# Kernel optimization log

Measured on AMD Instinct MI355X. Metric: run time of the kernel, lower is better.

## Reference

```python
import jax, jax.numpy as jnp
import numpy as np

B, L, D = 1, 256, 256
H, DK, R = 8, 32, 2
EPS = 1e-6


def _proj_ode(x, t, W, b, r):
    """Stand-in for ODELinear/InterpLinear: linear projection of x broadcast
    over a second time index with r exponential time-decay coefficients.
    x: [B,L,D], t: [B,L] -> [B,L,L,r,D_out]"""
    base = x @ W.T + b                                  # [B,L,Do]
    dt = jnp.abs(t[:, :, None] - t[:, None, :])         # [B,L,L]
    steps = jnp.linspace(0.0, 1.0, r, dtype=x.dtype)    # [r]
    coef = jnp.exp(-dt[:, :, :, None] * steps)          # [B,L,L,r]
    return coef[..., None] * base[:, None, :, None, :]  # [B,L,L,r,Do]


def _layer_norm(x, g, b):
    mu = x.mean(-1, keepdims=True)
    var = ((x - mu) ** 2).mean(-1, keepdims=True)
    return (x - mu) * jax.lax.rsqrt(var + EPS) * g + b


def setup_inputs() -> dict:
    key = jax.random.key(0)
    ks = jax.random.split(key, 12)
    s = 1.0 / np.sqrt(D)
    return {
        "q": jax.random.normal(ks[0], (B, L, D), jnp.float32),
        "k": jax.random.normal(ks[1], (B, L, D), jnp.float32),
        "v": jax.random.normal(ks[2], (B, L, D), jnp.float32),
        "t": jax.random.uniform(ks[3], (B, L), jnp.float32),
        "Wq": jax.random.normal(ks[4], (D, D), jnp.float32) * s,
        "bq": jnp.zeros((D,), jnp.float32),
        "Wk": jax.random.normal(ks[5], (D, D), jnp.float32) * s,
        "bk": jnp.zeros((D,), jnp.float32),
        "Wv": jax.random.normal(ks[6], (D, D), jnp.float32) * s,
        "bv": jnp.zeros((D,), jnp.float32),
        "fc_w": jax.random.normal(ks[7], (D, D), jnp.float32) * s,
        "fc_b": jnp.zeros((D,), jnp.float32),
        "ln_g": jnp.ones((D,), jnp.float32),
        "ln_b": jnp.zeros((D,), jnp.float32),
    }


def reference(q, k, v, t, Wq, bq, Wk, bk, Wv, bv, fc_w, fc_b, ln_g, ln_b):
    temp = DK ** 0.5
    residual = q
    qn = _layer_norm(q, ln_g, ln_b)  # normalize_before=True (only q)

    # [B,L,L,R,D] -> [B,L,L,R,H,DK] -> [B,H,L,L,R,DK]
    def to6(x):
        return x.reshape(B, L, L, R, H, DK).transpose(0, 4, 1, 2, 3, 5)

    qp = to6(_proj_ode(qn, t, Wq, bq, R))
    kp = to6(_proj_ode(k, t, Wk, bk, R))
    vp = to6(_proj_ode(v, t, Wv, bv, R))

    # attn = (q/temp * k).sum(-1).sum(-1): multiply-reduce over (R, DK), no matmul
    attn = jnp.einsum('bhijrd,bhijrd->bhij', qp, kp) / temp
    attn = jax.nn.softmax(attn, axis=-1)  # dropout=0 (eval)

    vs = vp.sum(axis=4)                                   # reduce R: [B,H,L,L,DK]
    out = jnp.einsum('bhij,bhijd->bhid', attn, vs)        # reduce second L
    out = out.transpose(0, 2, 1, 3).reshape(B, L, H * DK)
    out = out @ fc_w.T + fc_b
    out = out + residual
    return (out, attn)
```

## Files before the change

### kernel.cpp

```cpp
#include <hip/hip_runtime.h>
#include <math.h>


#define INV_TEMP 0.17677669529663687f

__device__ __forceinline__ void gemm_panel(
    const float* __restrict__ X, const float* __restrict__ W,
    const float* __restrict__ bias, const float* __restrict__ res,
    const float* __restrict__ ln_g, const float* __restrict__ ln_b,
    float* __restrict__ out, const int mode) {
  __shared__ float As[256][36];
  __shared__ float Bs[256][36];
  __shared__ float Red[4][32][36];
  const int t = threadIdx.x;
  const int j0 = blockIdx.y << 5, o0 = blockIdx.x << 5;
  const int lr = t >> 3;
  const int cg = (t & 7) << 2;
  float4 xa[8], wb[8];
#pragma unroll
  for (int u = 0; u < 8; ++u) {
    xa[u] = *(const float4*)(X + ((j0 + lr) << 8) + (u << 5) + cg);
    wb[u] = *(const float4*)(W + ((o0 + lr) << 8) + (u << 5) + cg);
  }
  if (mode == 0) {
    float s = 0.f, s2 = 0.f;
#pragma unroll
    for (int u = 0; u < 8; ++u) {
      s  += xa[u].x + xa[u].y + xa[u].z + xa[u].w;
      s2 += xa[u].x * xa[u].x + xa[u].y * xa[u].y +
            xa[u].z * xa[u].z + xa[u].w * xa[u].w;
    }
#pragma unroll
    for (int off = 1; off < 8; off <<= 1) {
      s  += __shfl_xor(s, off);
      s2 += __shfl_xor(s2, off);
    }
    const float mu = s * 0.00390625f;
    const float rs = rsqrtf(s2 * 0.00390625f - mu * mu + 1e-6f);
#pragma unroll
    for (int u = 0; u < 8; ++u) {
      const float4 gv = *(const float4*)(ln_g + (u << 5) + cg);
      const float4 bv = *(const float4*)(ln_b + (u << 5) + cg);
      xa[u].x = (xa[u].x - mu) * rs * gv.x + bv.x;
      xa[u].y = (xa[u].y - mu) * rs * gv.y + bv.y;
      xa[u].z = (xa[u].z - mu) * rs * gv.z + bv.z;
      xa[u].w = (xa[u].w - mu) * rs * gv.w + bv.w;
    }
  }
#pragma unroll
  for (int u = 0; u < 8; ++u) {
    const int c = (u << 5) + cg;
    As[c + 0][lr] = xa[u].x; As[c + 1][lr] = xa[u].y;
    As[c + 2][lr] = xa[u].z; As[c + 3][lr] = xa[u].w;
    Bs[c + 0][lr] = wb[u].x; Bs[c + 1][lr] = wb[u].y;
    Bs[c + 2][lr] = wb[u].z; Bs[c + 3][lr] = wb[u].w;
  }
  __syncthreads();

  const int w = t >> 6, lane = t & 63;
  const int jb = (lane >> 3) << 2;
  const int ob = (lane & 7) << 2;
  const int kbase = w << 6;
  float acc[4][4] = {{0.f}};
#pragma unroll 8
  for (int kk = 0; kk < 64; ++kk) {
    const float4 av = *(const float4*)&As[kbase + kk][jb];
    const float4 bv = *(const float4*)&Bs[kbase + kk][ob];
    acc[0][0] = fmaf(av.x, bv.x, acc[0][0]);
    acc[0][1] = fmaf(av.x, bv.y, acc[0][1]);
    acc[0][2] = fmaf(av.x, bv.z, acc[0][2]);
    acc[0][3] = fmaf(av.x, bv.w, acc[0][3]);
    acc[1][0] = fmaf(av.y, bv.x, acc[1][0]);
    acc[1][1] = fmaf(av.y, bv.y, acc[1][1]);
    acc[1][2] = fmaf(av.y, bv.z, acc[1][2]);
    acc[1][3] = fmaf(av.y, bv.w, acc[1][3]);
    acc[2][0] = fmaf(av.z, bv.x, acc[2][0]);
    acc[2][1] = fmaf(av.z, bv.y, acc[2][1]);
    acc[2][2] = fmaf(av.z, bv.z, acc[2][2]);
    acc[2][3] = fmaf(av.z, bv.w, acc[2][3]);
    acc[3][0] = fmaf(av.w, bv.x, acc[3][0]);
    acc[3][1] = fmaf(av.w, bv.y, acc[3][1]);
    acc[3][2] = fmaf(av.w, bv.z, acc[3][2]);
    acc[3][3] = fmaf(av.w, bv.w, acc[3][3]);
  }
#pragma unroll
  for (int r = 0; r < 4; ++r)
    *(float4*)&Red[w][jb + r][ob] =
        make_float4(acc[r][0], acc[r][1], acc[r][2], acc[r][3]);
  __syncthreads();

  const int j = t >> 3, o4 = (t & 7) << 2;
  const float4 s0 = *(const float4*)&Red[0][j][o4];
  const float4 s1 = *(const float4*)&Red[1][j][o4];
  const float4 s2 = *(const float4*)&Red[2][j][o4];
  const float4 s3 = *(const float4*)&Red[3][j][o4];
  const float4 bv4 = *(const float4*)(bias + o0 + o4);
  float4 rs4;
  rs4.x = (s0.x + s1.x) + (s2.x + s3.x) + bv4.x;
  rs4.y = (s0.y + s1.y) + (s2.y + s3.y) + bv4.y;
  rs4.z = (s0.z + s1.z) + (s2.z + s3.z) + bv4.z;
  rs4.w = (s0.w + s1.w) + (s2.w + s3.w) + bv4.w;
  const int gj = j0 + j, go = o0 + o4;
  if (mode <= 1) {
    out[((go + 0) << 8) + gj] = rs4.x;
    out[((go + 1) << 8) + gj] = rs4.y;
    out[((go + 2) << 8) + gj] = rs4.z;
    out[((go + 3) << 8) + gj] = rs4.w;
  } else {
    if (mode == 3) {
      const float4 rv = *(const float4*)(res + (gj << 8) + go);
      rs4.x += rv.x; rs4.y += rv.y; rs4.z += rv.z; rs4.w += rv.w;
    }
    *(float4*)(out + (gj << 8) + go) = rs4;
  }
}

__global__ __launch_bounds__(256) void mha_proj_gemm3(
    const float* __restrict__ q, const float* __restrict__ kin,
    const float* __restrict__ vin, const float* __restrict__ Wq,
    const float* __restrict__ bq, const float* __restrict__ Wk,
    const float* __restrict__ bk, const float* __restrict__ Wv,
    const float* __restrict__ bv, const float* __restrict__ ln_g,
    const float* __restrict__ ln_b, float* __restrict__ baseQT,
    float* __restrict__ baseKT, float* __restrict__ baseV) {
  const int z = blockIdx.z;
  if (z == 0)
    gemm_panel(q, Wq, bq, nullptr, ln_g, ln_b, baseQT, 0);
  else if (z == 1)
    gemm_panel(kin, Wk, bk, nullptr, nullptr, nullptr, baseKT, 1);
  else
    gemm_panel(vin, Wv, bv, nullptr, nullptr, nullptr, baseV, 2);
}

__global__ __launch_bounds__(256) void mha_fc_gemm(
    const float* __restrict__ ctxf, const float* __restrict__ fc_w,
    const float* __restrict__ fc_b, const float* __restrict__ q,
    float* __restrict__ out) {
  gemm_panel(ctxf, fc_w, fc_b, q, nullptr, nullptr, out, 3);
}

__global__ __launch_bounds__(512) void mha_attn_fused(
    const float* __restrict__ baseQT, const float* __restrict__ baseKT,
    const float* __restrict__ baseV, const float* __restrict__ tt,
    float* __restrict__ attn_out, float* __restrict__ ctxf) {
  const int h = blockIdx.y;
  const int i0 = blockIdx.x << 3;
  const int t = threadIdx.x;
  __shared__ float s_lds[256];
  __shared__ float P[8][256];
  if (t < 256) {
    const float* qc = baseQT + (h << 13) + t;
    const float* kc = baseKT + (h << 13) + t;
    float acc = 0.f;
#pragma unroll
    for (int dk = 0; dk < 32; ++dk)
      acc = fmaf(qc[dk << 8], kc[dk << 8], acc);
    s_lds[t] = acc * INV_TEMP;
  }
  __syncthreads();

  const int w = t >> 6, lane = t & 63;
  const int i = i0 + w;
  const float ti = tt[i];
  const float4 tj = ((const float4*)tt)[lane];
  const float4 sv = ((const float4*)s_lds)[lane];
  const float e0 = __expf(-fabsf(ti - tj.x));
  const float e1 = __expf(-fabsf(ti - tj.y));
  const float e2 = __expf(-fabsf(ti - tj.z));
  const float e3 = __expf(-fabsf(ti - tj.w));
  const float sc0 = (1.f + e0 * e0) * sv.x;
  const float sc1 = (1.f + e1 * e1) * sv.y;
  const float sc2 = (1.f + e2 * e2) * sv.z;
  const float sc3 = (1.f + e3 * e3) * sv.w;
  float m = fmaxf(fmaxf(sc0, sc1), fmaxf(sc2, sc3));
#pragma unroll
  for (int off = 32; off; off >>= 1) m = fmaxf(m, __shfl_xor(m, off));
  float p0 = __expf(sc0 - m), p1 = __expf(sc1 - m);
  float p2 = __expf(sc2 - m), p3 = __expf(sc3 - m);
  float s = p0 + p1 + p2 + p3;
#pragma unroll
  for (int off = 32; off; off >>= 1) s += __shfl_xor(s, off);
  const float rinv = 1.f / s;
  p0 *= rinv; p1 *= rinv; p2 *= rinv; p3 *= rinv;
  ((float4*)(attn_out + (((h << 8) + i) << 8)))[lane] =
      make_float4(p0, p1, p2, p3);
  ((float4*)P[w])[lane] = make_float4(p0 * (1.f + e0), p1 * (1.f + e1),
                                      p2 * (1.f + e2), p3 * (1.f + e3));

  const int dk = lane & 31, half = lane >> 5;
  const float* Pr = P[w] + (half << 7);
  const float* Vp = baseV + (h << 5) + dk + (half << 15);
  float a0 = 0.f, a1 = 0.f, a2 = 0.f, a3 = 0.f;
#pragma unroll 4
  for (int jj = 0; jj < 128; jj += 4) {
    a0 = fmaf(Pr[jj + 0], Vp[(jj + 0) << 8], a0);
    a1 = fmaf(Pr[jj + 1], Vp[(jj + 1) << 8], a1);
    a2 = fmaf(Pr[jj + 2], Vp[(jj + 2) << 8], a2);
    a3 = fmaf(Pr[jj + 3], Vp[(jj + 3) << 8], a3);
  }
  float acc = (a0 + a1) + (a2 + a3);
  acc += __shfl_xor(acc, 32);
  if (half == 0) ctxf[(i << 8) + (h << 5) + dk] = acc;
}

extern "C" void kernel_launch(void* const* d_in, const int* in_sizes, int n_in,
                              void* d_out, int out_size, void* d_ws,
                              size_t ws_size, hipStream_t stream) {
  const float* q    = (const float*)d_in[0];
  const float* kin  = (const float*)d_in[1];
  const float* vin  = (const float*)d_in[2];
  const float* tt   = (const float*)d_in[3];
  const float* Wq   = (const float*)d_in[4];
  const float* bq   = (const float*)d_in[5];
  const float* Wk   = (const float*)d_in[6];
  const float* bk   = (const float*)d_in[7];
  const float* Wv   = (const float*)d_in[8];
  const float* bv   = (const float*)d_in[9];
  const float* fc_w = (const float*)d_in[10];
  const float* fc_b = (const float*)d_in[11];
  const float* ln_g = (const float*)d_in[12];
  const float* ln_b = (const float*)d_in[13];

  float* out  = (float*)d_out;
  float* attn = out + 65536;

  float* ws     = (float*)d_ws;
  float* baseQT = ws;
  float* baseKT = ws + 65536;
  float* baseV  = ws + 131072;
  float* ctxf   = ws + 196608;

  hipLaunchKernelGGL(mha_proj_gemm3, dim3(8, 8, 3), dim3(256), 0, stream, q,
                     kin, vin, Wq, bq, Wk, bk, Wv, bv, ln_g, ln_b, baseQT,
                     baseKT, baseV);
  hipLaunchKernelGGL(mha_attn_fused, dim3(32, 8), dim3(512), 0, stream,
                     baseQT, baseKT, baseV, tt, attn, ctxf);
  hipLaunchKernelGGL(mha_fc_gemm, dim3(8, 8), dim3(256), 0, stream, ctxf,
                     fc_w, fc_b, q, out);
}
```

Baseline: 96.54 us.

## Fuse output projection into attention kernel with per-head atomic accumulation

Removes the separate fc GEMM launch. Each attention block now multiplies its per-head context slice by the matching rows of a transposed fc_w and atomically adds the partial result into the output. Head 0 also adds the bias and the residual. The projection kernel now zeroes the output and writes the fc_w transpose, so no extra launch is needed for that setup. This saves one kernel launch and the ctx round-trip through global memory. In exchange it adds eight float atomics per output element, which makes the summation order nondeterministic.

Measured after the change: 103.1 us. +6.8%, slower.

```diff
diff --git a/kernel.cpp b/kernel.cpp
--- a/kernel.cpp
+++ b/kernel.cpp
@@ -6,9 +6,8 @@
 
 __device__ __forceinline__ void gemm_panel(
     const float* __restrict__ X, const float* __restrict__ W,
-    const float* __restrict__ bias, const float* __restrict__ res,
-    const float* __restrict__ ln_g, const float* __restrict__ ln_b,
-    float* __restrict__ out, const int mode) {
+    const float* __restrict__ bias, const float* __restrict__ ln_g,
+    const float* __restrict__ ln_b, float* __restrict__ out, const int mode) {
   __shared__ float As[256][36];
   __shared__ float Bs[256][36];
   __shared__ float Red[4][32][36];
@@ -107,10 +106,6 @@
     out[((go + 2) << 8) + gj] = rs4.z;
     out[((go + 3) << 8) + gj] = rs4.w;
   } else {
-    if (mode == 3) {
-      const float4 rv = *(const float4*)(res + (gj << 8) + go);
-      rs4.x += rv.x; rs4.y += rv.y; rs4.z += rv.z; rs4.w += rv.w;
-    }
     *(float4*)(out + (gj << 8) + go) = rs4;
   }
 }
@@ -121,33 +116,45 @@
     const float* __restrict__ bq, const float* __restrict__ Wk,
     const float* __restrict__ bk, const float* __restrict__ Wv,
     const float* __restrict__ bv, const float* __restrict__ ln_g,
-    const float* __restrict__ ln_b, float* __restrict__ baseQT,
-    float* __restrict__ baseKT, float* __restrict__ baseV) {
+    const float* __restrict__ ln_b, const float* __restrict__ fc_w,
+    float* __restrict__ baseQT, float* __restrict__ baseKT,
+    float* __restrict__ baseV, float* __restrict__ fc_wT,
+    float* __restrict__ outz) {
   const int z = blockIdx.z;
+  const int gid = ((z << 6) + (blockIdx.y << 3) + blockIdx.x) * 256 +
+                  threadIdx.x;
+  if (gid < 16384)
+    ((float4*)outz)[gid] = make_float4(0.f, 0.f, 0.f, 0.f);
+  {
+    const int e = gid << 1;
+    if (e < 65536) {
+      const float2 v = *(const float2*)(fc_w + e);
+      const int o = e >> 8, d = e & 255;
+      fc_wT[(d << 8) + o] = v.x;
+      fc_wT[((d + 1 < 256 ? d + 1 : d - 255) << 8) +
+            (d + 1 < 256 ? o : o + 1)] = v.y;
+    }
+  }
   if (z == 0)
-    gemm_panel(q, Wq, bq, nullptr, ln_g, ln_b, baseQT, 0);
+    gemm_panel(q, Wq, bq, ln_g, ln_b, baseQT, 0);
   else if (z == 1)
-    gemm_panel(kin, Wk, bk, nullptr, nullptr, nullptr, baseKT, 1);
+    gemm_panel(kin, Wk, bk, nullptr, nullptr, baseKT, 1);
   else
-    gemm_panel(vin, Wv, bv, nullptr, nullptr, nullptr, baseV, 2);
-}
-
-__global__ __launch_bounds__(256) void mha_fc_gemm(
-    const float* __restrict__ ctxf, const float* __restrict__ fc_w,
-    const float* __restrict__ fc_b, const float* __restrict__ q,
-    float* __restrict__ out) {
-  gemm_panel(ctxf, fc_w, fc_b, q, nullptr, nullptr, out, 3);
-}
-
-__global__ __launch_bounds__(512) void mha_attn_fused(
+    gemm_panel(vin, Wv, bv, nullptr, nullptr, baseV, 2);
+}
+
+__global__ __launch_bounds__(512) void mha_attn_fc(
     const float* __restrict__ baseQT, const float* __restrict__ baseKT,
     const float* __restrict__ baseV, const float* __restrict__ tt,
-    float* __restrict__ attn_out, float* __restrict__ ctxf) {
+    const float* __restrict__ fc_wT, const float* __restrict__ fc_b,
+    const float* __restrict__ qres, float* __restrict__ attn_out,
+    float* __restrict__ out) {
   const int h = blockIdx.y;
   const int i0 = blockIdx.x << 3;
   const int t = threadIdx.x;
   __shared__ float s_lds[256];
   __shared__ float P[8][256];
+  __shared__ float ctx_lds[8][32];
   if (t < 256) {
     const float* qc = baseQT + (h << 13) + t;
     const float* kc = baseKT + (h << 13) + t;
@@ -200,7 +207,39 @@
   }
   float acc = (a0 + a1) + (a2 + a3);
   acc += __shfl_xor(acc, 32);
-  if (half == 0) ctxf[(i << 8) + (h << 5) + dk] = acc;
+  if (half == 0) ctx_lds[w][dk] = acc;
+  __syncthreads();
+
+  const int oq = lane << 2;
+  float4 c4[8];
+#pragma unroll
+  for (int u = 0; u < 8; ++u)
+    c4[u] = *(const float4*)&ctx_lds[w][u << 2];
+  const float* wt = fc_wT + (h << 13) + oq;
+  float4 acc4 = make_float4(0.f, 0.f, 0.f, 0.f);
+#pragma unroll
+  for (int u = 0; u < 8; ++u) {
+    const float4 cc = c4[u];
+    const float4 w0 = *(const float4*)(wt + ((u << 2) + 0 << 8));
+    const float4 w1 = *(const float4*)(wt + ((u << 2) + 1 << 8));
+    const float4 w2 = *(const float4*)(wt + ((u << 2) + 2 << 8));
+    const float4 w3 = *(const float4*)(wt + ((u << 2) + 3 << 8));
+    acc4.x = fmaf(cc.x, w0.x, fmaf(cc.y, w1.x, fmaf(cc.z, w2.x, fmaf(cc.w, w3.x, acc4.x))));
+    acc4.y = fmaf(cc.x, w0.y, fmaf(cc.y, w1.y, fmaf(cc.z, w2.y, fmaf(cc.w, w3.y, acc4.y))));
+    acc4.z = fmaf(cc.x, w0.z, fmaf(cc.y, w1.z, fmaf(cc.z, w2.z, fmaf(cc.w, w3.z, acc4.z))));
+    acc4.w = fmaf(cc.x, w0.w, fmaf(cc.y, w1.w, fmaf(cc.z, w2.w, fmaf(cc.w, w3.w, acc4.w))));
+  }
+  if (h == 0) {
+    const float4 bb = *(const float4*)(fc_b + oq);
+    const float4 rr = *(const float4*)(qres + (i << 8) + oq);
+    acc4.x += bb.x + rr.x; acc4.y += bb.y + rr.y;
+    acc4.z += bb.z + rr.z; acc4.w += bb.w + rr.w;
+  }
+  float* op = out + (i << 8) + oq;
+  unsafeAtomicAdd(op + 0, acc4.x);
+  unsafeAtomicAdd(op + 1, acc4.y);
+  unsafeAtomicAdd(op + 2, acc4.z);
+  unsafeAtomicAdd(op + 3, acc4.w);
 }
 
 extern "C" void kernel_launch(void* const* d_in, const int* in_sizes, int n_in,
@@ -228,13 +267,11 @@
   float* baseQT = ws;
   float* baseKT = ws + 65536;
   float* baseV  = ws + 131072;
-  float* ctxf   = ws + 196608;
+  float* fc_wT  = ws + 196608;
 
   hipLaunchKernelGGL(mha_proj_gemm3, dim3(8, 8, 3), dim3(256), 0, stream, q,
-                     kin, vin, Wq, bq, Wk, bk, Wv, bv, ln_g, ln_b, baseQT,
-                     baseKT, baseV);
-  hipLaunchKernelGGL(mha_attn_fused, dim3(32, 8), dim3(512), 0, stream,
-                     baseQT, baseKT, baseV, tt, attn, ctxf);
-  hipLaunchKernelGGL(mha_fc_gemm, dim3(8, 8), dim3(256), 0, stream, ctxf,
-                     fc_w, fc_b, q, out);
-}
+                     kin, vin, Wq, bq, Wk, bk, Wv, bv, ln_g, ln_b, fc_w,
+                     baseQT, baseKT, baseV, fc_wT, out);
+  hipLaunchKernelGGL(mha_attn_fc, dim3(32, 8), dim3(512), 0, stream, baseQT,
+                     baseKT, baseV, tt, fc_wT, fc_b, q, attn, out);
+}
```
